# Performance work log

Hardware: AMD Instinct MI355X
Metric: run time of the kernel (lower is better)

Reference implementation:

```python
import jax, jax.numpy as jnp
import numpy as np


def setup_inputs() -> dict:
    key = jax.random.key(0)
    ks = jax.random.split(key, 5)
    B, S, D, F, E = 4, 4096, 512, 2048, 8
    scale = 0.02
    return {
        "x": jax.random.normal(ks[0], (B, S, D), dtype=jnp.float32),
        "gate_w": jax.random.normal(ks[1], (E, D), dtype=jnp.float32) * scale,
        "w1": jax.random.normal(ks[2], (E, F, D), dtype=jnp.float32) * scale,
        "w2": jax.random.normal(ks[3], (E, D, F), dtype=jnp.float32) * scale,
        "w3": jax.random.normal(ks[4], (E, F, D), dtype=jnp.float32) * scale,
        "top_k": 2,
    }


def _moe(x, gate_w, w1, w2, w3, top_k):
    B, S, D = x.shape
    E = gate_w.shape[0]
    xt = x.reshape(-1, D)                       # [T, D], T = B*S
    T = xt.shape[0]

    # --- router: softmax in float32, top-k, renormalize (matches Mixtral) ---
    logits = xt @ gate_w.T                      # [T, E]
    probs = jax.nn.softmax(logits.astype(jnp.float32), axis=-1)
    rw, sel = jax.lax.top_k(probs, top_k)       # [T, k], [T, k]
    rw = rw / jnp.sum(rw, axis=-1, keepdims=True)
    rw = rw.astype(x.dtype)

    # dense combine weights [T, E]: zero for unselected experts
    combine = jnp.zeros((T, E), dtype=x.dtype)
    combine = combine.at[jnp.arange(T)[:, None], sel].add(rw)

    # --- per-expert SwiGLU-style FFN (relu gate), combined by routing weights ---
    out = jnp.zeros_like(xt)
    for e in range(E):  # small fixed expert count
        h = jax.nn.relu(xt @ w1[e].T) * (xt @ w3[e].T)   # [T, F]
        out = out + combine[:, e:e + 1] * (h @ w2[e].T)  # [T, D]
    return out.reshape(B, S, D)


def reference(x, gate_w, w1, w2, w3, top_k):
    return _moe(x, gate_w, w1, w2, w3, top_k)
```

## Files before the change

kernel.cpp:

```cpp
#include <hip/hip_runtime.h>
#include <stdint.h>

#define T_TOK 16384
#define D_DIM 512
#define F_DIM 2048
#define E_NUM 8
#define MAXR  34816

typedef __bf16 bf16x8 __attribute__((ext_vector_type(8)));
typedef float  f32x4  __attribute__((ext_vector_type(4)));

__device__ __forceinline__ unsigned short f2b(float f) {
  union { float f; unsigned u; } a; a.f = f;
  unsigned u = a.u;
  u = u + 0x7fffu + ((u >> 16) & 1u);
  return (unsigned short)(u >> 16);
}
__device__ __forceinline__ float b2f(unsigned short h) {
  union { unsigned u; float f; } a; a.u = ((unsigned)h) << 16;
  return a.f;
}
__device__ __forceinline__ void load_lds16(const void* g, void* l) {
  __builtin_amdgcn_global_load_lds(
      (const __attribute__((address_space(1))) void*)g,
      (__attribute__((address_space(3))) void*)l, 16, 0, 0);
}

#define CSTRIDE 16
#define BAR() __builtin_amdgcn_s_barrier()
#define SP1() __builtin_amdgcn_s_setprio(1)
#define SP0() __builtin_amdgcn_s_setprio(0)
#define VMC6() do { asm volatile("s_waitcnt vmcnt(6)" ::: "memory"); \
                    __builtin_amdgcn_sched_barrier(0); } while (0)
#define VMC2() do { asm volatile("s_waitcnt vmcnt(2)" ::: "memory"); \
                    __builtin_amdgcn_sched_barrier(0); } while (0)

__global__ __launch_bounds__(256) void router_kernel(
    const float* __restrict__ x, const float* __restrict__ gw,
    int* __restrict__ sel, float* __restrict__ rw)
{
  int lane = threadIdx.x & 63;
  int wid  = threadIdx.x >> 6;
  int t = blockIdx.x * 4 + wid;
  const float4* xp = (const float4*)(x + (size_t)t * D_DIM + lane * 8);
  float4 a0 = xp[0], a1 = xp[1];
  float lg[E_NUM];
#pragma unroll
  for (int e = 0; e < E_NUM; ++e) {
    const float4* gp = (const float4*)(gw + (size_t)e * D_DIM + lane * 8);
    float4 g0 = gp[0], g1 = gp[1];
    float s = a0.x*g0.x + a0.y*g0.y + a0.z*g0.z + a0.w*g0.w
            + a1.x*g1.x + a1.y*g1.y + a1.z*g1.z + a1.w*g1.w;
#pragma unroll
    for (int off = 32; off; off >>= 1) s += __shfl_xor(s, off);
    lg[e] = s;
  }
  if (lane == 0) {
    int i0 = 0; float m0 = lg[0];
#pragma unroll
    for (int e = 1; e < E_NUM; ++e) if (lg[e] > m0) { m0 = lg[e]; i0 = e; }
    int i1 = -1; float m1 = -1e30f;
#pragma unroll
    for (int e = 0; e < E_NUM; ++e) if (e != i0 && lg[e] > m1) { m1 = lg[e]; i1 = e; }
    float w0 = 1.0f / (1.0f + expf(m1 - m0));
    sel[2*t] = i0; sel[2*t+1] = i1;
    rw[2*t] = w0;  rw[2*t+1] = 1.0f - w0;
  }
}

__global__ __launch_bounds__(256) void hist_kernel(
    const int* __restrict__ sel, int* __restrict__ counts)
{
  __shared__ int h[E_NUM];
  if (threadIdx.x < E_NUM) h[threadIdx.x] = 0;
  __syncthreads();
  int t = blockIdx.x * 256 + threadIdx.x;
  atomicAdd(&h[sel[2*t]], 1);
  atomicAdd(&h[sel[2*t+1]], 1);
  __syncthreads();
  if (threadIdx.x < E_NUM) atomicAdd(&counts[threadIdx.x * CSTRIDE], h[threadIdx.x]);
}

__global__ void scan_kernel(const int* __restrict__ counts, int* __restrict__ offs,
    int* __restrict__ padTot)
{
  if (threadIdx.x != 0 || blockIdx.x != 0) return;
  int o = 0;
  for (int e = 0; e < E_NUM; ++e) {
    offs[e] = o;
    o += (counts[e * CSTRIDE] + 255) & ~255;
  }
  *padTot = o;
}

__global__ __launch_bounds__(256) void padfill_kernel(
    const int* __restrict__ counts, const int* __restrict__ offs,
    int* __restrict__ ptok, float* __restrict__ pw, int* __restrict__ pexp)
{
  int e = blockIdx.x;
  int c = counts[e * CSTRIDE];
  int o = offs[e];
  int padded = (c + 255) & ~255;
  for (int i = c + threadIdx.x; i < padded; i += 256) {
    ptok[o+i] = 0; pw[o+i] = 0.0f; pexp[o+i] = e;
  }
}

__global__ __launch_bounds__(256) void assign_kernel(
    const int* __restrict__ sel, const float* __restrict__ rw,
    const int* __restrict__ offs, int* __restrict__ cursor,
    int* __restrict__ ptok, float* __restrict__ pw, int* __restrict__ pexp,
    int* __restrict__ t2s)
{
  __shared__ int lcnt[E_NUM];
  __shared__ int base[E_NUM];
  if (threadIdx.x < E_NUM) lcnt[threadIdx.x] = 0;
  __syncthreads();
  int t = blockIdx.x * 256 + threadIdx.x;
  int e[2], rank[2];
  float w[2];
#pragma unroll
  for (int k = 0; k < 2; ++k) {
    e[k] = sel[2*t+k];
    w[k] = rw[2*t+k];
    rank[k] = atomicAdd(&lcnt[e[k]], 1);
  }
  __syncthreads();
  if (threadIdx.x < E_NUM)
    base[threadIdx.x] = atomicAdd(&cursor[threadIdx.x * CSTRIDE], lcnt[threadIdx.x]);
  __syncthreads();
#pragma unroll
  for (int k = 0; k < 2; ++k) {
    int slot = offs[e[k]] + base[e[k]] + rank[k];
    ptok[slot] = t; pw[slot] = w[k]; pexp[slot] = e[k];
    t2s[2*t+k] = slot;
  }
}

__global__ __launch_bounds__(256) void cvt4_kernel(
    const float* __restrict__ s0, const float* __restrict__ s1,
    const float* __restrict__ s2, const float* __restrict__ s3,
    unsigned short* __restrict__ d0, unsigned short* __restrict__ d1,
    unsigned short* __restrict__ d2, unsigned short* __restrict__ d3)
{
  int seg = blockIdx.x >> 13;
  int i = (blockIdx.x & 8191) * 256 + threadIdx.x;
  const float* s = seg == 0 ? s0 : seg == 1 ? s1 : seg == 2 ? s2 : s3;
  unsigned short* d = seg == 0 ? d0 : seg == 1 ? d1 : seg == 2 ? d2 : d3;
  float4 v = ((const float4*)s)[i];
  ushort4 o;
  o.x = f2b(v.x); o.y = f2b(v.y); o.z = f2b(v.z); o.w = f2b(v.w);
  ((ushort4*)d)[i] = o;
}


__device__ __forceinline__ void stageA8(unsigned short* dst, const unsigned short* xb,
    const int* tokr, int kt, int half, int tid, int csw) {
  int k0 = kt * 64;
#pragma unroll
  for (int r = 0; r < 2; ++r) {
    int h = half*2 + r;
    int rl = h*64 + (tid>>3);
    load_lds16(xb + (size_t)tokr[h]*D_DIM + k0 + csw, &dst[rl*64 + (tid&7)*8]);
  }
}
__device__ __forceinline__ void stageB8(unsigned short* dst, const unsigned short* W,
    int f0, int kt, int tid, int csw) {
  int k0 = kt * 64;
#pragma unroll
  for (int r = 0; r < 2; ++r) {
    int rl = r*64 + (tid>>3);
    load_lds16(W + (size_t)(f0+rl)*D_DIM + k0 + csw, &dst[rl*64 + (tid&7)*8]);
  }
}
__device__ __forceinline__ void readA8(bf16x8 (*af)[2], const unsigned short* buf,
    int wm, int lane, int xs, int mlo) {
#pragma unroll
  for (int m = 0; m < 4; ++m)
#pragma unroll
    for (int s = 0; s < 2; ++s)
      af[m][s] = *(const bf16x8*)&buf[(wm*128 + (mlo+m)*16 + (lane&15))*64 + ((s*32 + ((lane>>4)<<3)) ^ xs)];
}
__device__ __forceinline__ void readB8(bf16x8 (*bf)[2], const unsigned short* buf,
    int wn, int lane, int xs) {
#pragma unroll
  for (int n = 0; n < 2; ++n)
#pragma unroll
    for (int s = 0; s < 2; ++s)
      bf[n][s] = *(const bf16x8*)&buf[(wn*32 + n*16 + (lane&15))*64 + ((s*32 + ((lane>>4)<<3)) ^ xs)];
}
__device__ __forceinline__ void mfmaq(f32x4 (*acc)[2], const bf16x8 (*af)[2], const bf16x8 (*bf)[2]) {
#pragma unroll
  for (int m = 0; m < 4; ++m)
#pragma unroll
    for (int n = 0; n < 2; ++n)
#pragma unroll
      for (int s = 0; s < 2; ++s)
        acc[m][n] = __builtin_amdgcn_mfma_f32_16x16x32_bf16(af[m][s], bf[n][s], acc[m][n], 0, 0, 0);
}

__global__ __launch_bounds__(512, 2) void ffn_h8_kernel(
    const unsigned short* __restrict__ xb, const unsigned short* __restrict__ w1b,
    const unsigned short* __restrict__ w3b, const int* __restrict__ ptok,
    const int* __restrict__ pexp, const int* __restrict__ padTot,
    unsigned short* __restrict__ H)
{
  __shared__ unsigned short As0[256*64], As1[256*64];
  __shared__ unsigned short B1s0[128*64], B1s1[128*64];
  __shared__ unsigned short B3s0[128*64], B3s1[128*64];
  int tm = blockIdx.x >> 4;
  int tn = blockIdx.x & 15;
  int row0 = tm * 256;
  if (row0 >= *padTot) return;
  int e  = pexp[row0];
  int f0 = tn * 128;
  const unsigned short* W1 = w1b + (size_t)e * F_DIM * D_DIM;
  const unsigned short* W3 = w3b + (size_t)e * F_DIM * D_DIM;
  int tid  = threadIdx.x;
  int lane = tid & 63;
  int wid  = tid >> 6;
  int wm = wid >> 2, wn = wid & 3;
  int xs  = (lane & 7) << 3;
  int csw = ((tid & 7) ^ ((tid >> 3) & 7)) * 8;

  int tokr[4];
#pragma unroll
  for (int h = 0; h < 4; ++h) tokr[h] = ptok[row0 + h*64 + (tid>>3)];

  f32x4 acc1[8][2] = {};
  f32x4 acc3[8][2] = {};
  bf16x8 afL[4][2], afH[4][2], b1f[2][2], b3f[2][2];

  stageB8(B1s0, W1, f0, 0, tid, csw);
  stageA8(As0, xb, tokr, 0, 0, tid, csw);
  stageA8(As0, xb, tokr, 0, 1, tid, csw);
  stageB8(B3s0, W3, f0, 0, tid, csw);
  stageB8(B1s1, W1, f0, 1, tid, csw);
  stageA8(As1, xb, tokr, 1, 0, tid, csw);
  stageA8(As1, xb, tokr, 1, 1, tid, csw);
  VMC6();
  BAR();

  for (int i = 0; i < 4; ++i) {
    int ktB = 2*i + 1;
    int s2 = (2*i + 2 < 8) ? 2*i + 2 : 6;
    int s3 = (2*i + 3 < 8) ? 2*i + 3 : 7;
    readA8(afL, As0, wm, lane, xs, 0);
    readB8(b1f, B1s0, wn, lane, xs);
    stageB8(B3s1, W3, f0, ktB, tid, csw);
    BAR(); mfmaq(&acc1[0], afL, b1f); BAR();
    readA8(afH, As0, wm, lane, xs, 4);
    stageB8(B1s0, W1, f0, s2, tid, csw);
    BAR(); mfmaq(&acc1[4], afH, b1f); BAR();
    readB8(b3f, B3s0, wn, lane, xs);
    stageA8(As0, xb, tokr, s2, 0, tid, csw);
    BAR(); mfmaq(&acc3[0], afL, b3f); BAR();
    stageA8(As0, xb, tokr, s2, 1, tid, csw);
    VMC6();
    BAR(); mfmaq(&acc3[4], afH, b3f); BAR();
    readA8(afL, As1, wm, lane, xs, 0);
    readB8(b1f, B1s1, wn, lane, xs);
    stageB8(B3s0, W3, f0, s2, tid, csw);
    BAR(); mfmaq(&acc1[0], afL, b1f); BAR();
    readA8(afH, As1, wm, lane, xs, 4);
    stageB8(B1s1, W1, f0, s3, tid, csw);
    BAR(); mfmaq(&acc1[4], afH, b1f); BAR();
    readB8(b3f, B3s1, wn, lane, xs);
    stageA8(As1, xb, tokr, s3, 0, tid, csw);
    BAR(); mfmaq(&acc3[0], afL, b3f); BAR();
    stageA8(As1, xb, tokr, s3, 1, tid, csw);
    VMC6();
    BAR(); mfmaq(&acc3[4], afH, b3f); BAR();
  }

#pragma unroll
  for (int mi = 0; mi < 8; ++mi) {
    int rbase = row0 + wm*128 + mi*16 + (lane>>4)*4;
#pragma unroll
    for (int ni = 0; ni < 2; ++ni) {
      int col = f0 + wn*32 + ni*16 + (lane & 15);
#pragma unroll
      for (int j = 0; j < 4; ++j) {
        float h = fmaxf(acc1[mi][ni][j], 0.0f) * acc3[mi][ni][j];
        H[(size_t)(rbase + j) * F_DIM + col] = f2b(h);
      }
    }
  }
}

__device__ __forceinline__ void stageA_O(unsigned short* dst, const unsigned short* H,
    int row0, int kt, int tid, int csw) {
  int k0 = kt * 64;
#pragma unroll
  for (int r = 0; r < 2; ++r) {
    int rl = r*64 + (tid>>3);
    load_lds16(H + (size_t)(row0+rl)*F_DIM + k0 + csw, &dst[rl*64 + (tid&7)*8]);
  }
}
__device__ __forceinline__ void stageB_O(unsigned short* d1, unsigned short* d3,
    const unsigned short* W2, int d0, int kt, int tid, int csw) {
  int k0 = kt * 64;
  int rl = tid >> 3;
  load_lds16(W2 + (size_t)(d0+rl)*F_DIM + k0 + csw, &d1[rl*64 + (tid&7)*8]);
  load_lds16(W2 + (size_t)(d0+64+rl)*F_DIM + k0 + csw, &d3[rl*64 + (tid&7)*8]);
}
__device__ __forceinline__ void readA_O(bf16x8 (*af)[2], const unsigned short* buf,
    int wm, int lane, int xs) {
#pragma unroll
  for (int m = 0; m < 4; ++m)
#pragma unroll
    for (int s = 0; s < 2; ++s)
      af[m][s] = *(const bf16x8*)&buf[(wm*64 + m*16 + (lane&15))*64 + ((s*32 + ((lane>>4)<<3)) ^ xs)];
}
__device__ __forceinline__ void readB_O(bf16x8* bf, const unsigned short* buf,
    int wn, int lane, int xs) {
#pragma unroll
  for (int s = 0; s < 2; ++s)
    bf[s] = *(const bf16x8*)&buf[(wn*16 + (lane&15))*64 + ((s*32 + ((lane>>4)<<3)) ^ xs)];
}
__device__ __forceinline__ void mfmaO(f32x4* acc, const bf16x8 (*af)[2], const bf16x8* bf) {
  SP1();
#pragma unroll
  for (int m = 0; m < 4; ++m)
#pragma unroll
    for (int s = 0; s < 2; ++s)
      acc[m] = __builtin_amdgcn_mfma_f32_16x16x32_bf16(af[m][s], bf[s], acc[m], 0, 0, 0);
  SP0();
}

__global__ __launch_bounds__(512, 4) void ffn_out8_kernel(
    const unsigned short* __restrict__ H, const unsigned short* __restrict__ w2b,
    const int* __restrict__ pexp, const float* __restrict__ pw,
    const int* __restrict__ padTot, unsigned short* __restrict__ contrib)
{
  __shared__ unsigned short As0[128*64], As1[128*64];
  __shared__ unsigned short B1s0[64*64], B1s1[64*64];
  __shared__ unsigned short B3s0[64*64], B3s1[64*64];
  int wgid = (blockIdx.x & 7) * 136 + (blockIdx.x >> 3);
  int tm = wgid >> 2;
  int tn = wgid & 3;
  int row0 = tm * 128;
  if (row0 >= *padTot) return;
  int e  = pexp[row0];
  int d0 = tn * 128;
  const unsigned short* W2 = w2b + (size_t)e * D_DIM * F_DIM;
  int tid  = threadIdx.x;
  int lane = tid & 63;
  int wid  = tid >> 6;
  int wm = wid >> 2, wn = wid & 3;
  int xs  = (lane & 7) << 3;
  int csw = ((tid & 7) ^ ((tid >> 3) & 7)) * 8;

  f32x4 acc1[4] = {};
  f32x4 acc3[4] = {};
  bf16x8 af[4][2], b1f[2], b3f[2];

  const int NK = F_DIM / 64;
  stageA_O(As0, H, row0, 0, tid, csw);
  stageB_O(B1s0, B3s0, W2, d0, 0, tid, csw);
  stageA_O(As1, H, row0, 1, tid, csw);
  VMC2();
  BAR();

  for (int i = 0; i < NK/2; ++i) {
    int k1 = 2*i + 1;
    int k2 = (2*i + 2 < NK) ? 2*i + 2 : NK - 1;
    int k3 = (2*i + 3 < NK) ? 2*i + 3 : NK - 1;
    readA_O(af, As0, wm, lane, xs);
    readB_O(b1f, B1s0, wn, lane, xs);
    readB_O(b3f, B3s0, wn, lane, xs);
    stageB_O(B1s1, B3s1, W2, d0, k1, tid, csw);
    BAR(); mfmaO(acc1, af, b1f); BAR();
    stageA_O(As0, H, row0, k2, tid, csw);
    VMC2();
    BAR(); mfmaO(acc3, af, b3f); BAR();
    readA_O(af, As1, wm, lane, xs);
    readB_O(b1f, B1s1, wn, lane, xs);
    readB_O(b3f, B3s1, wn, lane, xs);
    stageB_O(B1s0, B3s0, W2, d0, k2, tid, csw);
    BAR(); mfmaO(acc1, af, b1f); BAR();
    stageA_O(As1, H, row0, k3, tid, csw);
    VMC2();
    BAR(); mfmaO(acc3, af, b3f); BAR();
  }

#pragma unroll
  for (int m = 0; m < 4; ++m) {
    int rbase = row0 + wm*64 + m*16 + (lane>>4)*4;
    float sw[4];
#pragma unroll
    for (int j = 0; j < 4; ++j) sw[j] = pw[rbase + j];
    int colL = d0 + wn*16 + (lane & 15);
#pragma unroll
    for (int j = 0; j < 4; ++j) {
      contrib[(size_t)(rbase + j) * D_DIM + colL]      = f2b(acc1[m][j] * sw[j]);
      contrib[(size_t)(rbase + j) * D_DIM + colL + 64] = f2b(acc3[m][j] * sw[j]);
    }
  }
}

__global__ __launch_bounds__(256) void combine_kernel(
    const unsigned short* __restrict__ contrib, const int* __restrict__ t2s,
    float* __restrict__ out)
{
  int i = blockIdx.x * 256 + threadIdx.x;
  int t = i >> 7;
  int c = (i & 127) * 4;
  int s0 = t2s[2*t], s1 = t2s[2*t+1];
  ushort4 u0 = *(const ushort4*)&contrib[(size_t)s0 * D_DIM + c];
  ushort4 u1 = *(const ushort4*)&contrib[(size_t)s1 * D_DIM + c];
  float4 o;
  o.x = b2f(u0.x) + b2f(u1.x);
  o.y = b2f(u0.y) + b2f(u1.y);
  o.z = b2f(u0.z) + b2f(u1.z);
  o.w = b2f(u0.w) + b2f(u1.w);
  *(float4*)&out[(size_t)t * D_DIM + c] = o;
}

#define OFF_SEL   ((size_t)2048)
#define OFF_RW    (OFF_SEL  + (size_t)2*T_TOK*4)
#define OFF_T2S   (OFF_RW   + (size_t)2*T_TOK*4)
#define OFF_PTOK  (OFF_T2S  + (size_t)2*T_TOK*4)
#define OFF_PW    (OFF_PTOK + (size_t)MAXR*4)
#define OFF_PEXP  (OFF_PW   + (size_t)MAXR*4)
#define OFF_XB    (OFF_PEXP + (size_t)MAXR*4)
#define OFF_W1B   (OFF_XB   + (size_t)T_TOK*D_DIM*2)
#define OFF_W3B   (OFF_W1B  + (size_t)E_NUM*F_DIM*D_DIM*2)
#define OFF_W2B   (OFF_W3B  + (size_t)E_NUM*F_DIM*D_DIM*2)
#define OFF_H     (OFF_W2B  + (size_t)E_NUM*F_DIM*D_DIM*2)
#define OFF_CONTR OFF_XB

extern "C" void kernel_launch(void* const* d_in, const int* in_sizes, int n_in,
                              void* d_out, int out_size, void* d_ws, size_t ws_size,
                              hipStream_t stream) {
  const float* x  = (const float*)d_in[0];
  const float* gw = (const float*)d_in[1];
  const float* w1 = (const float*)d_in[2];
  const float* w2 = (const float*)d_in[3];
  const float* w3 = (const float*)d_in[4];
  float* out = (float*)d_out;
  char* ws = (char*)d_ws;

  int*   counts = (int*)(ws + 0);
  int*   cursor = (int*)(ws + 512);
  int*   offs   = (int*)(ws + 1024);
  int*   padTot = (int*)(ws + 1056);
  int*   sel    = (int*)(ws + OFF_SEL);
  float* rw     = (float*)(ws + OFF_RW);
  int*   t2s    = (int*)(ws + OFF_T2S);
  int*   ptok   = (int*)(ws + OFF_PTOK);
  float* pw     = (float*)(ws + OFF_PW);
  int*   pexp   = (int*)(ws + OFF_PEXP);
  unsigned short* xb      = (unsigned short*)(ws + OFF_XB);
  unsigned short* w1b     = (unsigned short*)(ws + OFF_W1B);
  unsigned short* w3b     = (unsigned short*)(ws + OFF_W3B);
  unsigned short* w2b     = (unsigned short*)(ws + OFF_W2B);
  unsigned short* Hbuf    = (unsigned short*)(ws + OFF_H);
  unsigned short* contrib = (unsigned short*)(ws + OFF_CONTR);

  hipMemsetAsync(ws, 0, 2048, stream);

  cvt4_kernel<<<4 * 8192, 256, 0, stream>>>(x, w1, w3, w2, xb, w1b, w3b, w2b);

  router_kernel<<<T_TOK/4, 256, 0, stream>>>(x, gw, sel, rw);
  hist_kernel<<<T_TOK/256, 256, 0, stream>>>(sel, counts);
  scan_kernel<<<1, 64, 0, stream>>>(counts, offs, padTot);
  padfill_kernel<<<E_NUM, 256, 0, stream>>>(counts, offs, ptok, pw, pexp);
  assign_kernel<<<T_TOK/256, 256, 0, stream>>>(sel, rw, offs, cursor, ptok, pw, pexp, t2s);

  ffn_h8_kernel<<<(MAXR/256)*(F_DIM/128), 512, 0, stream>>>(xb, w1b, w3b, ptok, pexp, padTot, Hbuf);
  ffn_out8_kernel<<<(MAXR/128)*(D_DIM/128), 512, 0, stream>>>(Hbuf, w2b, pexp, pw, padTot, contrib);
  combine_kernel<<<(T_TOK*D_DIM/4)/256, 256, 0, stream>>>(contrib, t2s, out);

  (void)in_sizes; (void)n_in; (void)out_size; (void)ws_size;
}
```

Baseline: 320.7 us.

## Shrink gate/up FFN tile to 128x64 with XCD swizzle; fuse x bf16 cast into router

The gate/up FFN kernel moves from 256x128 tiles at two blocks per CU to 128x64 tiles at four blocks per CU. It reuses the down-projection kernel's fragment and MFMA helpers and adds a block-index swizzle that groups work across XCDs. The x float-to-bf16 conversion moves into the router kernel, which already reads x, so the separate cast kernel only handles the three weight tensors. The smaller tiles give more parallelism and occupancy but lower arithmetic intensity, so each block reloads activations and weights more often.

```diff
diff --git a/kernel.cpp b/kernel.cpp
--- a/kernel.cpp
+++ b/kernel.cpp
@@ -30,20 +30,24 @@
 #define BAR() __builtin_amdgcn_s_barrier()
 #define SP1() __builtin_amdgcn_s_setprio(1)
 #define SP0() __builtin_amdgcn_s_setprio(0)
-#define VMC6() do { asm volatile("s_waitcnt vmcnt(6)" ::: "memory"); \
-                    __builtin_amdgcn_sched_barrier(0); } while (0)
 #define VMC2() do { asm volatile("s_waitcnt vmcnt(2)" ::: "memory"); \
                     __builtin_amdgcn_sched_barrier(0); } while (0)
 
 __global__ __launch_bounds__(256) void router_kernel(
     const float* __restrict__ x, const float* __restrict__ gw,
-    int* __restrict__ sel, float* __restrict__ rw)
+    int* __restrict__ sel, float* __restrict__ rw, unsigned short* __restrict__ xb)
 {
   int lane = threadIdx.x & 63;
   int wid  = threadIdx.x >> 6;
   int t = blockIdx.x * 4 + wid;
   const float4* xp = (const float4*)(x + (size_t)t * D_DIM + lane * 8);
   float4 a0 = xp[0], a1 = xp[1];
+  ushort4 o0, o1;
+  o0.x = f2b(a0.x); o0.y = f2b(a0.y); o0.z = f2b(a0.z); o0.w = f2b(a0.w);
+  o1.x = f2b(a1.x); o1.y = f2b(a1.y); o1.z = f2b(a1.z); o1.w = f2b(a1.w);
+  ushort4* xbp = (ushort4*)(xb + (size_t)t * D_DIM + lane * 8);
+  xbp[0] = o0; xbp[1] = o1;
+
   float lg[E_NUM];
 #pragma unroll
   for (int e = 0; e < E_NUM; ++e) {
@@ -137,16 +141,16 @@
   }
 }
 
-__global__ __launch_bounds__(256) void cvt4_kernel(
+__global__ __launch_bounds__(256) void cvt3_kernel(
     const float* __restrict__ s0, const float* __restrict__ s1,
-    const float* __restrict__ s2, const float* __restrict__ s3,
+    const float* __restrict__ s2,
     unsigned short* __restrict__ d0, unsigned short* __restrict__ d1,
-    unsigned short* __restrict__ d2, unsigned short* __restrict__ d3)
+    unsigned short* __restrict__ d2)
 {
   int seg = blockIdx.x >> 13;
   int i = (blockIdx.x & 8191) * 256 + threadIdx.x;
-  const float* s = seg == 0 ? s0 : seg == 1 ? s1 : seg == 2 ? s2 : s3;
-  unsigned short* d = seg == 0 ? d0 : seg == 1 ? d1 : seg == 2 ? d2 : d3;
+  const float* s = seg == 0 ? s0 : seg == 1 ? s1 : s2;
+  unsigned short* d = seg == 0 ? d0 : seg == 1 ? d1 : d2;
   float4 v = ((const float4*)s)[i];
   ushort4 o;
   o.x = f2b(v.x); o.y = f2b(v.y); o.z = f2b(v.z); o.w = f2b(v.w);
@@ -154,66 +158,63 @@
 }
 
 
-__device__ __forceinline__ void stageA8(unsigned short* dst, const unsigned short* xb,
-    const int* tokr, int kt, int half, int tid, int csw) {
-  int k0 = kt * 64;
-#pragma unroll
-  for (int r = 0; r < 2; ++r) {
-    int h = half*2 + r;
-    int rl = h*64 + (tid>>3);
-    load_lds16(xb + (size_t)tokr[h]*D_DIM + k0 + csw, &dst[rl*64 + (tid&7)*8]);
-  }
-}
-__device__ __forceinline__ void stageB8(unsigned short* dst, const unsigned short* W,
-    int f0, int kt, int tid, int csw) {
+__device__ __forceinline__ void readA_O(bf16x8 (*af)[2], const unsigned short* buf,
+    int wm, int lane, int xs) {
+#pragma unroll
+  for (int m = 0; m < 4; ++m)
+#pragma unroll
+    for (int s = 0; s < 2; ++s)
+      af[m][s] = *(const bf16x8*)&buf[(wm*64 + m*16 + (lane&15))*64 + ((s*32 + ((lane>>4)<<3)) ^ xs)];
+}
+__device__ __forceinline__ void readB_O(bf16x8* bf, const unsigned short* buf,
+    int wn, int lane, int xs) {
+#pragma unroll
+  for (int s = 0; s < 2; ++s)
+    bf[s] = *(const bf16x8*)&buf[(wn*16 + (lane&15))*64 + ((s*32 + ((lane>>4)<<3)) ^ xs)];
+}
+__device__ __forceinline__ void mfmaO(f32x4* acc, const bf16x8 (*af)[2], const bf16x8* bf) {
+  SP1();
+#pragma unroll
+  for (int m = 0; m < 4; ++m)
+#pragma unroll
+    for (int s = 0; s < 2; ++s)
+      acc[m] = __builtin_amdgcn_mfma_f32_16x16x32_bf16(af[m][s], bf[s], acc[m], 0, 0, 0);
+  SP0();
+}
+
+__device__ __forceinline__ void stageA_H(unsigned short* dst, const unsigned short* xb,
+    const int* tokr, int kt, int tid, int csw) {
   int k0 = kt * 64;
 #pragma unroll
   for (int r = 0; r < 2; ++r) {
     int rl = r*64 + (tid>>3);
-    load_lds16(W + (size_t)(f0+rl)*D_DIM + k0 + csw, &dst[rl*64 + (tid&7)*8]);
-  }
-}
-__device__ __forceinline__ void readA8(bf16x8 (*af)[2], const unsigned short* buf,
-    int wm, int lane, int xs, int mlo) {
-#pragma unroll
-  for (int m = 0; m < 4; ++m)
-#pragma unroll
-    for (int s = 0; s < 2; ++s)
-      af[m][s] = *(const bf16x8*)&buf[(wm*128 + (mlo+m)*16 + (lane&15))*64 + ((s*32 + ((lane>>4)<<3)) ^ xs)];
-}
-__device__ __forceinline__ void readB8(bf16x8 (*bf)[2], const unsigned short* buf,
-    int wn, int lane, int xs) {
-#pragma unroll
-  for (int n = 0; n < 2; ++n)
-#pragma unroll
-    for (int s = 0; s < 2; ++s)
-      bf[n][s] = *(const bf16x8*)&buf[(wn*32 + n*16 + (lane&15))*64 + ((s*32 + ((lane>>4)<<3)) ^ xs)];
-}
-__device__ __forceinline__ void mfmaq(f32x4 (*acc)[2], const bf16x8 (*af)[2], const bf16x8 (*bf)[2]) {
-#pragma unroll
-  for (int m = 0; m < 4; ++m)
-#pragma unroll
-    for (int n = 0; n < 2; ++n)
-#pragma unroll
-      for (int s = 0; s < 2; ++s)
-        acc[m][n] = __builtin_amdgcn_mfma_f32_16x16x32_bf16(af[m][s], bf[n][s], acc[m][n], 0, 0, 0);
-}
-
-__global__ __launch_bounds__(512, 2) void ffn_h8_kernel(
+    load_lds16(xb + (size_t)tokr[r]*D_DIM + k0 + csw, &dst[rl*64 + (tid&7)*8]);
+  }
+}
+__device__ __forceinline__ void stageB_H(unsigned short* d1, unsigned short* d3,
+    const unsigned short* W1, const unsigned short* W3, int f0, int kt, int tid, int csw) {
+  int k0 = kt * 64;
+  int rl = tid >> 3;
+  load_lds16(W1 + (size_t)(f0+rl)*D_DIM + k0 + csw, &d1[rl*64 + (tid&7)*8]);
+  load_lds16(W3 + (size_t)(f0+rl)*D_DIM + k0 + csw, &d3[rl*64 + (tid&7)*8]);
+}
+
+__global__ __launch_bounds__(512, 4) void ffn_h64_kernel(
     const unsigned short* __restrict__ xb, const unsigned short* __restrict__ w1b,
     const unsigned short* __restrict__ w3b, const int* __restrict__ ptok,
     const int* __restrict__ pexp, const int* __restrict__ padTot,
     unsigned short* __restrict__ H)
 {
-  __shared__ unsigned short As0[256*64], As1[256*64];
-  __shared__ unsigned short B1s0[128*64], B1s1[128*64];
-  __shared__ unsigned short B3s0[128*64], B3s1[128*64];
-  int tm = blockIdx.x >> 4;
-  int tn = blockIdx.x & 15;
-  int row0 = tm * 256;
+  __shared__ unsigned short As0[128*64], As1[128*64];
+  __shared__ unsigned short B1s0[64*64], B1s1[64*64];
+  __shared__ unsigned short B3s0[64*64], B3s1[64*64];
+  int wgid = (blockIdx.x & 7) * 1088 + (blockIdx.x >> 3);
+  int tm = wgid >> 5;
+  int tn = wgid & 31;
+  int row0 = tm * 128;
   if (row0 >= *padTot) return;
   int e  = pexp[row0];
-  int f0 = tn * 128;
+  int f0 = tn * 64;
   const unsigned short* W1 = w1b + (size_t)e * F_DIM * D_DIM;
   const unsigned short* W3 = w3b + (size_t)e * F_DIM * D_DIM;
   int tid  = threadIdx.x;
@@ -223,67 +224,51 @@
   int xs  = (lane & 7) << 3;
   int csw = ((tid & 7) ^ ((tid >> 3) & 7)) * 8;
 
-  int tokr[4];
-#pragma unroll
-  for (int h = 0; h < 4; ++h) tokr[h] = ptok[row0 + h*64 + (tid>>3)];
-
-  f32x4 acc1[8][2] = {};
-  f32x4 acc3[8][2] = {};
-  bf16x8 afL[4][2], afH[4][2], b1f[2][2], b3f[2][2];
-
-  stageB8(B1s0, W1, f0, 0, tid, csw);
-  stageA8(As0, xb, tokr, 0, 0, tid, csw);
-  stageA8(As0, xb, tokr, 0, 1, tid, csw);
-  stageB8(B3s0, W3, f0, 0, tid, csw);
-  stageB8(B1s1, W1, f0, 1, tid, csw);
-  stageA8(As1, xb, tokr, 1, 0, tid, csw);
-  stageA8(As1, xb, tokr, 1, 1, tid, csw);
-  VMC6();
+  int tokr[2];
+#pragma unroll
+  for (int r = 0; r < 2; ++r) tokr[r] = ptok[row0 + r*64 + (tid>>3)];
+
+  f32x4 acc1[4] = {};
+  f32x4 acc3[4] = {};
+  bf16x8 af[4][2], b1f[2], b3f[2];
+
+  const int NK = D_DIM / 64;
+  stageA_H(As0, xb, tokr, 0, tid, csw);
+  stageB_H(B1s0, B3s0, W1, W3, f0, 0, tid, csw);
+  stageA_H(As1, xb, tokr, 1, tid, csw);
+  VMC2();
   BAR();
 
-  for (int i = 0; i < 4; ++i) {
-    int ktB = 2*i + 1;
-    int s2 = (2*i + 2 < 8) ? 2*i + 2 : 6;
-    int s3 = (2*i + 3 < 8) ? 2*i + 3 : 7;
-    readA8(afL, As0, wm, lane, xs, 0);
-    readB8(b1f, B1s0, wn, lane, xs);
-    stageB8(B3s1, W3, f0, ktB, tid, csw);
-    BAR(); mfmaq(&acc1[0], afL, b1f); BAR();
-    readA8(afH, As0, wm, lane, xs, 4);
-    stageB8(B1s0, W1, f0, s2, tid, csw);
-    BAR(); mfmaq(&acc1[4], afH, b1f); BAR();
-    readB8(b3f, B3s0, wn, lane, xs);
-    stageA8(As0, xb, tokr, s2, 0, tid, csw);
-    BAR(); mfmaq(&acc3[0], afL, b3f); BAR();
-    stageA8(As0, xb, tokr, s2, 1, tid, csw);
-    VMC6();
-    BAR(); mfmaq(&acc3[4], afH, b3f); BAR();
-    readA8(afL, As1, wm, lane, xs, 0);
-    readB8(b1f, B1s1, wn, lane, xs);
-    stageB8(B3s0, W3, f0, s2, tid, csw);
-    BAR(); mfmaq(&acc1[0], afL, b1f); BAR();
-    readA8(afH, As1, wm, lane, xs, 4);
-    stageB8(B1s1, W1, f0, s3, tid, csw);
-    BAR(); mfmaq(&acc1[4], afH, b1f); BAR();
-    readB8(b3f, B3s1, wn, lane, xs);
-    stageA8(As1, xb, tokr, s3, 0, tid, csw);
-    BAR(); mfmaq(&acc3[0], afL, b3f); BAR();
-    stageA8(As1, xb, tokr, s3, 1, tid, csw);
-    VMC6();
-    BAR(); mfmaq(&acc3[4], afH, b3f); BAR();
-  }
-
-#pragma unroll
-  for (int mi = 0; mi < 8; ++mi) {
-    int rbase = row0 + wm*128 + mi*16 + (lane>>4)*4;
-#pragma unroll
-    for (int ni = 0; ni < 2; ++ni) {
-      int col = f0 + wn*32 + ni*16 + (lane & 15);
-#pragma unroll
-      for (int j = 0; j < 4; ++j) {
-        float h = fmaxf(acc1[mi][ni][j], 0.0f) * acc3[mi][ni][j];
-        H[(size_t)(rbase + j) * F_DIM + col] = f2b(h);
-      }
+  for (int i = 0; i < NK/2; ++i) {
+    int k1 = 2*i + 1;
+    int k2 = (2*i + 2 < NK) ? 2*i + 2 : NK - 1;
+    int k3 = (2*i + 3 < NK) ? 2*i + 3 : NK - 1;
+    readA_O(af, As0, wm, lane, xs);
+    readB_O(b1f, B1s0, wn, lane, xs);
+    readB_O(b3f, B3s0, wn, lane, xs);
+    stageB_H(B1s1, B3s1, W1, W3, f0, k1, tid, csw);
+    BAR(); mfmaO(acc1, af, b1f); BAR();
+    stageA_H(As0, xb, tokr, k2, tid, csw);
+    VMC2();
+    BAR(); mfmaO(acc3, af, b3f); BAR();
+    readA_O(af, As1, wm, lane, xs);
+    readB_O(b1f, B1s1, wn, lane, xs);
+    readB_O(b3f, B3s1, wn, lane, xs);
+    stageB_H(B1s0, B3s0, W1, W3, f0, k2, tid, csw);
+    BAR(); mfmaO(acc1, af, b1f); BAR();
+    stageA_H(As1, xb, tokr, k3, tid, csw);
+    VMC2();
+    BAR(); mfmaO(acc3, af, b3f); BAR();
+  }
+
+#pragma unroll
+  for (int m = 0; m < 4; ++m) {
+    int rbase = row0 + wm*64 + m*16 + (lane>>4)*4;
+    int col = f0 + wn*16 + (lane & 15);
+#pragma unroll
+    for (int j = 0; j < 4; ++j) {
+      float h = fmaxf(acc1[m][j], 0.0f) * acc3[m][j];
+      H[(size_t)(rbase + j) * F_DIM + col] = f2b(h);
     }
   }
 }
@@ -303,29 +288,6 @@
   int rl = tid >> 3;
   load_lds16(W2 + (size_t)(d0+rl)*F_DIM + k0 + csw, &d1[rl*64 + (tid&7)*8]);
   load_lds16(W2 + (size_t)(d0+64+rl)*F_DIM + k0 + csw, &d3[rl*64 + (tid&7)*8]);
-}
-__device__ __forceinline__ void readA_O(bf16x8 (*af)[2], const unsigned short* buf,
-    int wm, int lane, int xs) {
-#pragma unroll
-  for (int m = 0; m < 4; ++m)
-#pragma unroll
-    for (int s = 0; s < 2; ++s)
-      af[m][s] = *(const bf16x8*)&buf[(wm*64 + m*16 + (lane&15))*64 + ((s*32 + ((lane>>4)<<3)) ^ xs)];
-}
-__device__ __forceinline__ void readB_O(bf16x8* bf, const unsigned short* buf,
-    int wn, int lane, int xs) {
-#pragma unroll
-  for (int s = 0; s < 2; ++s)
-    bf[s] = *(const bf16x8*)&buf[(wn*16 + (lane&15))*64 + ((s*32 + ((lane>>4)<<3)) ^ xs)];
-}
-__device__ __forceinline__ void mfmaO(f32x4* acc, const bf16x8 (*af)[2], const bf16x8* bf) {
-  SP1();
-#pragma unroll
-  for (int m = 0; m < 4; ++m)
-#pragma unroll
-    for (int s = 0; s < 2; ++s)
-      acc[m] = __builtin_amdgcn_mfma_f32_16x16x32_bf16(af[m][s], bf[s], acc[m], 0, 0, 0);
-  SP0();
 }
 
 __global__ __launch_bounds__(512, 4) void ffn_out8_kernel(
@@ -460,15 +422,15 @@
 
   hipMemsetAsync(ws, 0, 2048, stream);
 
-  cvt4_kernel<<<4 * 8192, 256, 0, stream>>>(x, w1, w3, w2, xb, w1b, w3b, w2b);
-
-  router_kernel<<<T_TOK/4, 256, 0, stream>>>(x, gw, sel, rw);
+  cvt3_kernel<<<3 * 8192, 256, 0, stream>>>(w1, w3, w2, w1b, w3b, w2b);
+
+  router_kernel<<<T_TOK/4, 256, 0, stream>>>(x, gw, sel, rw, xb);
   hist_kernel<<<T_TOK/256, 256, 0, stream>>>(sel, counts);
   scan_kernel<<<1, 64, 0, stream>>>(counts, offs, padTot);
   padfill_kernel<<<E_NUM, 256, 0, stream>>>(counts, offs, ptok, pw, pexp);
   assign_kernel<<<T_TOK/256, 256, 0, stream>>>(sel, rw, offs, cursor, ptok, pw, pexp, t2s);
 
-  ffn_h8_kernel<<<(MAXR/256)*(F_DIM/128), 512, 0, stream>>>(xb, w1b, w3b, ptok, pexp, padTot, Hbuf);
+  ffn_h64_kernel<<<(MAXR/128)*(F_DIM/64), 512, 0, stream>>>(xb, w1b, w3b, ptok, pexp, padTot, Hbuf);
   ffn_out8_kernel<<<(MAXR/128)*(D_DIM/128), 512, 0, stream>>>(Hbuf, w2b, pexp, pw, padTot, contrib);
   combine_kernel<<<(T_TOK*D_DIM/4)/256, 256, 0, stream>>>(contrib, t2s, out);
 
```

Result: slower. 334.2 us (+4.2%).
